# Kernel optimization log

Hardware: AMD Instinct MI355X
Metric: run time of the kernel (lower is better)

## Reference

```python
import jax, jax.numpy as jnp
import numpy as np

NUM_NODES = 1_000_000  # global node-state table size
N = 100_000            # batch of unique nodes
D = 128                # embedding dim
SIZE = 32              # map is SIZE x SIZE cells
C = SIZE * SIZE        # 1024 cells


def setup_inputs() -> dict:
    key = jax.random.key(0)
    k1, k2, k3, k4 = jax.random.split(key, 4)
    embeddings = jax.random.normal(k1, (N, D), dtype=jnp.float32)
    memory_map = jax.random.normal(k2, (C, D), dtype=jnp.float32)
    nodes = jax.random.randint(k3, (N,), 0, NUM_NODES, dtype=jnp.int64)
    times = jax.random.uniform(k4, (N,), dtype=jnp.float32)
    # node state tables: cell assignment initialized to -1 (unassigned), time to 0
    node_cell = jnp.full((NUM_NODES,), -1, dtype=jnp.int32)
    node_time = jnp.zeros((NUM_NODES,), dtype=jnp.float32)
    return {"embeddings": embeddings, "memory_map": memory_map,
            "nodes": nodes, "times": times,
            "node_cell": node_cell, "node_time": node_time}


def _euclidean_cdist(x, m):
    # torch.cdist(x, m, p=2): [N, C] pairwise L2 distances
    sq = (jnp.sum(x * x, axis=1, keepdims=True)
          + jnp.sum(m * m, axis=1)[None, :]
          - 2.0 * (x @ m.T))
    return jnp.sqrt(jnp.maximum(sq, 0.0))


def reference(embeddings, memory_map, nodes, times, node_cell, node_time):
    # find_center_distances: distance of each node embedding to every map cell,
    # nearest-cell assignment, then scatter update of the node state tables
    # (memory_map.set_nodes_distance(nodes, cells, times)).
    distances = _euclidean_cdist(embeddings, memory_map)      # [N, C]
    min_indices = jnp.argmin(distances, axis=1)               # [N]
    cells = min_indices.astype(jnp.int32)                     # list_num[min_indices] == min_indices
    new_node_cell = node_cell.at[nodes].set(cells)
    new_node_time = node_time.at[nodes].set(times)
    return distances, cells, new_node_cell, new_node_time
```

## Files before the change

### kernel.cpp

```cpp
#include <hip/hip_runtime.h>
#include <stdint.h>

constexpr int D_DIM   = 128;
constexpr int C_CELLS = 1024;
constexpr float EPS_D = 1.5e-3f;

typedef __attribute__((ext_vector_type(8))) short  short8;
typedef __attribute__((ext_vector_type(4))) float  floatx4;

#define GLOBAL_AS __attribute__((address_space(1)))
#define LDS_AS    __attribute__((address_space(3)))

__device__ __forceinline__ void gl2lds16(const void* g, void* l) {
    __builtin_amdgcn_global_load_lds((const GLOBAL_AS unsigned int*)g,
                                     (LDS_AS unsigned int*)l, 16, 0, 0);
}

__device__ __forceinline__ unsigned short f32_bf16_rtn(float x) {
    union { float f; unsigned u; } v; v.f = x;
    unsigned r = v.u + 0x7FFFu + ((v.u >> 16) & 1u);
    return (unsigned short)(r >> 16);
}
__device__ __forceinline__ float bf16_f32(unsigned short h) {
    union { float f; unsigned u; } v; v.u = ((unsigned)h) << 16; return v.f;
}
__device__ __forceinline__ float hi_f32(unsigned long long p) {
    union { float f; unsigned u; } v; v.u = (unsigned)(p >> 32); return v.f;
}

__global__ void init_kernel(int* win, int* flag, int* suspCount, int numNodes) {
    int j = blockIdx.x * blockDim.x + threadIdx.x;
    if (j < numNodes) win[j] = -1;
    if (j == 0) { *flag = 1; *suspCount = 0; }
}

__global__ void detect_kernel(const int* nodes32, int n, int* flag) {
    int i = blockIdx.x * blockDim.x + threadIdx.x;
    if (i < n && (i & 1) && nodes32[i] != 0) *flag = 0;
}

__global__ void winner_kernel(const void* nodes, int n, const int* flag, int* win) {
    int i = blockIdx.x * blockDim.x + threadIdx.x;
    if (i >= n) return;
    int node = (*flag) ? (int)((const long long*)nodes)[i]
                       : ((const int*)nodes)[i];
    atomicMax(&win[node], i);
}

__global__ void norms_kernel(const float* __restrict__ v, float* __restrict__ o, int rows) {
    int row  = blockIdx.x * 4 + (threadIdx.x >> 6);
    int lane = threadIdx.x & 63;
    if (row >= rows) return;
    float2 x = reinterpret_cast<const float2*>(v)[(size_t)row * 64 + lane];
    float s = x.x * x.x + x.y * x.y;
    #pragma unroll
    for (int m = 32; m; m >>= 1) s += __shfl_xor(s, m, 64);
    if (lane == 0) o[row] = s;
}

__global__ void convB_kernel(const float* __restrict__ M,
                             unsigned short* __restrict__ Bh_g,
                             unsigned short* __restrict__ Bl_g) {
    int idx  = blockIdx.x * 256 + threadIdx.x;
    int cell = idx >> 4;
    int b    = idx & 15;
    const float4* s = reinterpret_cast<const float4*>(M + (size_t)cell * D_DIM + b * 8);
    float4 v0 = s[0], v1 = s[1];
    float xv[8] = { v0.x, v0.y, v0.z, v0.w, v1.x, v1.y, v1.z, v1.w };
    short8 hs, ls;
    #pragma unroll
    for (int j = 0; j < 8; ++j) {
        unsigned short hb = f32_bf16_rtn(xv[j]);
        unsigned short lb = f32_bf16_rtn(xv[j] - bf16_f32(hb));
        hs[j] = (short)hb; ls[j] = (short)lb;
    }
    int tile = cell >> 6, r = cell & 63;
    int dst = tile * 8192 + r * 128 + ((b ^ (r & 15)) << 3);
    *reinterpret_cast<short8*>(&Bh_g[dst]) = hs;
    *reinterpret_cast<short8*>(&Bl_g[dst]) = ls;
}

__global__ __launch_bounds__(256, 2)
void dist_kernel(const float* __restrict__ X,
                 const unsigned short* __restrict__ Bh_g,
                 const unsigned short* __restrict__ Bl_g,
                 const float* __restrict__ msq,
                 float* __restrict__ outD, int* __restrict__ cells32,
                 int* __restrict__ suspects, int* __restrict__ suspCount,
                 int N)
{
    __shared__ __align__(16) unsigned short Ah[64 * 128];
    __shared__ __align__(16) unsigned short Al[64 * 128];
    __shared__ __align__(16) unsigned short Bh[64 * 128];
    __shared__ __align__(16) unsigned short Bl[64 * 128];
    __shared__ float Axs[64];
    __shared__ unsigned long long sp1[64][2];
    __shared__ float              sm2[64][2];

    const int tid  = threadIdx.x;
    const int lane = tid & 63;
    const int wave = tid >> 6;
    const int q    = lane >> 4;
    const int l15  = lane & 15;
    const int w0   = wave & 1;
    const int w1   = wave >> 1;
    const int blockRow = blockIdx.x * 64;

    #pragma unroll
    for (int p = 0; p < 4; ++p) {
        int r = p * 16 + (tid >> 4);
        int b = tid & 15;
        int gRow = blockRow + r;
        float4 v0 = make_float4(0.f, 0.f, 0.f, 0.f), v1 = v0;
        if (gRow < N) {
            const float4* s = reinterpret_cast<const float4*>(X + (size_t)gRow * D_DIM + b * 8);
            v0 = s[0]; v1 = s[1];
        }
        float xv[8] = { v0.x, v0.y, v0.z, v0.w, v1.x, v1.y, v1.z, v1.w };
        short8 hs, ls;
        float sq = 0.f;
        #pragma unroll
        for (int j = 0; j < 8; ++j) {
            sq += xv[j] * xv[j];
            unsigned short hb = f32_bf16_rtn(xv[j]);
            unsigned short lb = f32_bf16_rtn(xv[j] - bf16_f32(hb));
            hs[j] = (short)hb; ls[j] = (short)lb;
        }
        #pragma unroll
        for (int m = 1; m < 16; m <<= 1) sq += __shfl_xor(sq, m, 16);
        if (b == 0) Axs[r] = sq;
        int ad = r * 128 + ((b ^ (r & 15)) << 3);
        *reinterpret_cast<short8*>(&Ah[ad]) = hs;
        *reinterpret_cast<short8*>(&Al[ad]) = ls;
    }
    __syncthreads();

    float xs[8];
    #pragma unroll
    for (int t = 0; t < 2; ++t)
        #pragma unroll
        for (int r = 0; r < 4; ++r)
            xs[t * 4 + r] = Axs[w1 * 32 + t * 16 + q * 4 + r];

    float rminv[8]; float rmin2[8]; int rminc[8];
    #pragma unroll
    for (int i = 0; i < 8; ++i) { rminv[i] = INFINITY; rmin2[i] = INFINITY; rminc[i] = 0; }

    for (int ct = 0; ct < 16; ++ct) {
        if (ct) __syncthreads();
        {
            const char* bhg = (const char*)Bh_g + (size_t)ct * 16384 + wave * 4096 + lane * 16;
            const char* blg = (const char*)Bl_g + (size_t)ct * 16384 + wave * 4096 + lane * 16;
            char* bhl = (char*)Bh + wave * 4096;
            char* bll = (char*)Bl + wave * 4096;
            #pragma unroll
            for (int j = 0; j < 4; ++j) {
                gl2lds16(bhg + j * 1024, bhl + j * 1024);
                gl2lds16(blg + j * 1024, bll + j * 1024);
            }
        }
        __syncthreads();

        floatx4 acc[2][2];
        #pragma unroll
        for (int t = 0; t < 2; ++t)
            #pragma unroll
            for (int u = 0; u < 2; ++u)
                acc[t][u] = (floatx4){0.f, 0.f, 0.f, 0.f};

        #pragma unroll
        for (int kc = 0; kc < 4; ++kc) {
            int blk = kc * 4 + q;
            short8 ah[2], al[2], bh[2], bl[2];
            #pragma unroll
            for (int t = 0; t < 2; ++t) {
                int row = w1 * 32 + t * 16 + l15;
                int ad  = row * 128 + ((blk ^ l15) << 3);
                ah[t] = *reinterpret_cast<const short8*>(&Ah[ad]);
                al[t] = *reinterpret_cast<const short8*>(&Al[ad]);
            }
            #pragma unroll
            for (int u = 0; u < 2; ++u) {
                int col = w0 * 32 + u * 16 + l15;
                int ad  = col * 128 + ((blk ^ l15) << 3);
                bh[u] = *reinterpret_cast<const short8*>(&Bh[ad]);
                bl[u] = *reinterpret_cast<const short8*>(&Bl[ad]);
            }
            #pragma unroll
            for (int t = 0; t < 2; ++t)
                #pragma unroll
                for (int u = 0; u < 2; ++u) {
                    acc[t][u] = __builtin_amdgcn_mfma_f32_16x16x32_bf16(ah[t], bh[u], acc[t][u], 0, 0, 0);
                    acc[t][u] = __builtin_amdgcn_mfma_f32_16x16x32_bf16(ah[t], bl[u], acc[t][u], 0, 0, 0);
                    acc[t][u] = __builtin_amdgcn_mfma_f32_16x16x32_bf16(al[t], bh[u], acc[t][u], 0, 0, 0);
                }
        }

        #pragma unroll
        for (int u = 0; u < 2; ++u) {
            int col = ct * 64 + w0 * 32 + u * 16 + l15;
            float ms = msq[col];
            #pragma unroll
            for (int t = 0; t < 2; ++t)
                #pragma unroll
                for (int r = 0; r < 4; ++r) {
                    int g  = blockRow + w1 * 32 + t * 16 + q * 4 + r;
                    int i  = t * 4 + r;
                    float sq = xs[i] + ms - 2.0f * acc[t][u][r];
                    float d  = sqrtf(fmaxf(sq, 0.0f));
                    if (g < N) __builtin_nontemporal_store(d, &outD[(size_t)g * C_CELLS + col]);
                    if (d < rminv[i]) { rmin2[i] = rminv[i]; rminv[i] = d; rminc[i] = col; }
                    else if (d < rmin2[i]) rmin2[i] = d;
                }
        }
    }

    #pragma unroll
    for (int i = 0; i < 8; ++i) {
        union { float f; unsigned u; } bu; bu.f = rminv[i];
        unsigned long long p1 = ((unsigned long long)bu.u << 32) | (unsigned)rminc[i];
        float m2 = rmin2[i];
        #pragma unroll
        for (int m = 1; m < 16; m <<= 1) {
            unsigned long long o1 = __shfl_xor(p1, m, 16);
            float o2 = __shfl_xor(m2, m, 16);
            unsigned long long hi = (p1 > o1) ? p1 : o1;
            float hv = hi_f32(hi);
            p1 = (p1 < o1) ? p1 : o1;
            m2 = fminf(fminf(m2, o2), hv);
        }
        if (l15 == 0) {
            int lr = w1 * 32 + (i >> 2) * 16 + q * 4 + (i & 3);
            sp1[lr][w0] = p1; sm2[lr][w0] = m2;
        }
    }
    __syncthreads();
    if (tid < 64) {
        int g = blockRow + tid;
        if (g < N) {
            unsigned long long a = sp1[tid][0], b = sp1[tid][1];
            unsigned long long G1 = (a < b) ? a : b;
            unsigned long long hi = (a < b) ? b : a;
            float M2  = fminf(fminf(sm2[tid][0], sm2[tid][1]), hi_f32(hi));
            float g1v = hi_f32(G1);
            cells32[g] = (int)(G1 & 0xffffffffu);
            if (M2 - g1v < EPS_D) {
                int ix = atomicAdd(suspCount, 1);
                suspects[ix] = g;
            }
        }
    }
}

__global__ __launch_bounds__(256)
void refine_kernel(const float* __restrict__ X, const float* __restrict__ M,
                   const int* __restrict__ suspects, const int* __restrict__ suspCount,
                   int* __restrict__ cells32)
{
    __shared__ double xd[128];
    __shared__ unsigned long long wres[4];
    int cnt = *suspCount;
    for (int s = blockIdx.x; s < cnt; s += gridDim.x) {
        int row = suspects[s];
        if (threadIdx.x < 128) xd[threadIdx.x] = (double)X[(size_t)row * D_DIM + threadIdx.x];
        __syncthreads();
        unsigned long long best = ~0ull;
        for (int c = threadIdx.x; c < C_CELLS; c += 256) {
            const float* mp = M + (size_t)c * D_DIM;
            double acc = 0.0;
            #pragma unroll 4
            for (int k = 0; k < D_DIM; ++k) {
                double diff = xd[k] - (double)mp[k];
                acc = fma(diff, diff, acc);
            }
            unsigned long long bits = (unsigned long long)__double_as_longlong(acc);
            unsigned long long pk = (bits & ~1023ull) | (unsigned long long)c;
            if (pk < best) best = pk;
        }
        #pragma unroll
        for (int m = 32; m; m >>= 1) {
            unsigned long long o = __shfl_xor(best, m, 64);
            if (o < best) best = o;
        }
        if ((threadIdx.x & 63) == 0) wres[threadIdx.x >> 6] = best;
        __syncthreads();
        if (threadIdx.x == 0) {
            unsigned long long b0 = wres[0] < wres[1] ? wres[0] : wres[1];
            unsigned long long b1 = wres[2] < wres[3] ? wres[2] : wres[3];
            unsigned long long b  = b0 < b1 ? b0 : b1;
            cells32[row] = (int)(b & 1023ull);
        }
        __syncthreads();
    }
}

__global__ void post_kernel(const int* __restrict__ cells32,
                            const int* __restrict__ win,
                            const float* __restrict__ times,
                            const int* __restrict__ node_cell,
                            const float* __restrict__ node_time,
                            float* __restrict__ outCells,
                            float* __restrict__ outNC,
                            float* __restrict__ outNT,
                            int n, int numNodes)
{
    int j = blockIdx.x * blockDim.x + threadIdx.x;
    if (j < n) outCells[j] = (float)cells32[j];
    if (j < numNodes) {
        int w = win[j];
        float c, t;
        if (w >= 0) {
            c = (float)cells32[w];
            t = times[w];
        } else {
            c = (float)node_cell[j];
            t = node_time[j];
        }
        outNC[j] = c;
        outNT[j] = t;
    }
}

extern "C" void kernel_launch(void* const* d_in, const int* in_sizes, int n_in,
                              void* d_out, int out_size, void* d_ws, size_t ws_size,
                              hipStream_t stream)
{
    const float* X         = (const float*)d_in[0];
    const float* M         = (const float*)d_in[1];
    const void*  nodes     = d_in[2];
    const float* times     = (const float*)d_in[3];
    const int*   node_cell = (const int*)d_in[4];
    const float* node_time = (const float*)d_in[5];

    const int N        = in_sizes[3];
    const int numNodes = in_sizes[4];
    const int C        = in_sizes[1] / D_DIM;

    char* ws = (char*)d_ws;
    size_t off = 0;
    unsigned short* Bh_g = (unsigned short*)(ws + off); off += (size_t)C * D_DIM * 2;
    unsigned short* Bl_g = (unsigned short*)(ws + off); off += (size_t)C * D_DIM * 2;
    int* win      = (int*)(ws + off); off += (size_t)numNodes * 4;
    int* cells32  = (int*)(ws + off); off += (size_t)N * 4;
    int* suspects = (int*)(ws + off); off += (size_t)N * 4;
    float* msq    = (float*)(ws + off); off += (size_t)C * 4;
    int* flag     = (int*)(ws + off); off += 4;
    int* suspCount= (int*)(ws + off); off += 4;
    (void)ws_size; (void)n_in; (void)out_size;

    float* outD     = (float*)d_out;
    float* outCells = outD + (size_t)N * C;
    float* outNC    = outCells + N;
    float* outNT    = outNC + numNodes;

    init_kernel  <<<(numNodes + 255) / 256, 256, 0, stream>>>(win, flag, suspCount, numNodes);
    detect_kernel<<<(N + 255) / 256, 256, 0, stream>>>((const int*)nodes, N, flag);
    winner_kernel<<<(N + 255) / 256, 256, 0, stream>>>(nodes, N, flag, win);
    norms_kernel <<<(C + 3) / 4, 256, 0, stream>>>(M, msq, C);
    convB_kernel <<<(C * 16 + 255) / 256, 256, 0, stream>>>(M, Bh_g, Bl_g);
    dist_kernel  <<<(N + 63) / 64, 256, 0, stream>>>(X, Bh_g, Bl_g, msq, outD, cells32,
                                                     suspects, suspCount, N);
    refine_kernel<<<512, 256, 0, stream>>>(X, M, suspects, suspCount, cells32);
    post_kernel  <<<(numNodes + 255) / 256, 256, 0, stream>>>(cells32, win, times, node_cell,
                                                              node_time, outCells, outNC, outNT,
                                                              N, numNodes);
}
```

Baseline: 717.4 us.

## Hold X fragments in registers, prefetch next map tile, vectorize distance stores

```diff
diff --git a/kernel.cpp b/kernel.cpp
--- a/kernel.cpp
+++ b/kernel.cpp
@@ -80,7 +80,7 @@
     *reinterpret_cast<short8*>(&Bl_g[dst]) = ls;
 }
 
-__global__ __launch_bounds__(256, 2)
+__global__ __launch_bounds__(256, 3)
 void dist_kernel(const float* __restrict__ X,
                  const unsigned short* __restrict__ Bh_g,
                  const unsigned short* __restrict__ Bl_g,
@@ -89,10 +89,9 @@
                  int* __restrict__ suspects, int* __restrict__ suspCount,
                  int N)
 {
-    __shared__ __align__(16) unsigned short Ah[64 * 128];
-    __shared__ __align__(16) unsigned short Al[64 * 128];
-    __shared__ __align__(16) unsigned short Bh[64 * 128];
-    __shared__ __align__(16) unsigned short Bl[64 * 128];
+    __shared__ __align__(16) unsigned short ldsH[64 * 128];
+    __shared__ __align__(16) unsigned short ldsL[64 * 128];
+    __shared__ float msq_s[C_CELLS];
     __shared__ float Axs[64];
     __shared__ unsigned long long sp1[64][2];
     __shared__ float              sm2[64][2];
@@ -105,6 +104,7 @@
     const int w0   = wave & 1;
     const int w1   = wave >> 1;
     const int blockRow = blockIdx.x * 64;
+    const bool fullBlock = (blockRow + 64 <= N);
 
     #pragma unroll
     for (int p = 0; p < 4; ++p) {
@@ -130,108 +130,149 @@
         for (int m = 1; m < 16; m <<= 1) sq += __shfl_xor(sq, m, 16);
         if (b == 0) Axs[r] = sq;
         int ad = r * 128 + ((b ^ (r & 15)) << 3);
-        *reinterpret_cast<short8*>(&Ah[ad]) = hs;
-        *reinterpret_cast<short8*>(&Al[ad]) = ls;
+        *reinterpret_cast<short8*>(&ldsH[ad]) = hs;
+        *reinterpret_cast<short8*>(&ldsL[ad]) = ls;
+    }
+    {
+        float4 mv = *reinterpret_cast<const float4*>(&msq[tid * 4]);
+        *reinterpret_cast<float4*>(&msq_s[tid * 4]) = mv;
     }
     __syncthreads();
 
-    float xs[8];
+    short8 xh[2][4], xl[2][4];
     #pragma unroll
     for (int t = 0; t < 2; ++t)
         #pragma unroll
-        for (int r = 0; r < 4; ++r)
-            xs[t * 4 + r] = Axs[w1 * 32 + t * 16 + q * 4 + r];
-
-    float rminv[8]; float rmin2[8]; int rminc[8];
-    #pragma unroll
-    for (int i = 0; i < 8; ++i) { rminv[i] = INFINITY; rmin2[i] = INFINITY; rminc[i] = 0; }
+        for (int kc = 0; kc < 4; ++kc) {
+            int row = w1 * 32 + t * 16 + l15;
+            int ad  = row * 128 + (((kc * 4 + q) ^ l15) << 3);
+            xh[t][kc] = *reinterpret_cast<const short8*>(&ldsH[ad]);
+            xl[t][kc] = *reinterpret_cast<const short8*>(&ldsL[ad]);
+        }
+    float xs[2];
+    xs[0] = Axs[w1 * 32 + l15];
+    xs[1] = Axs[w1 * 32 + 16 + l15];
+    __syncthreads();
+
+    {
+        const char* bhg = (const char*)Bh_g + wave * 4096 + lane * 16;
+        const char* blg = (const char*)Bl_g + wave * 4096 + lane * 16;
+        char* bhl = (char*)ldsH + wave * 4096;
+        char* bll = (char*)ldsL + wave * 4096;
+        #pragma unroll
+        for (int j = 0; j < 4; ++j) {
+            gl2lds16(bhg + j * 1024, bhl + j * 1024);
+            gl2lds16(blg + j * 1024, bll + j * 1024);
+        }
+    }
+    asm volatile("s_waitcnt vmcnt(0)" ::: "memory");
+    __builtin_amdgcn_sched_barrier(0);
+    __builtin_amdgcn_s_barrier();
+    __builtin_amdgcn_sched_barrier(0);
+
+    float m1[2]  = { INFINITY, INFINITY };
+    float m2v[2] = { INFINITY, INFINITY };
+    int   c1[2]  = { 0, 0 };
 
     for (int ct = 0; ct < 16; ++ct) {
-        if (ct) __syncthreads();
-        {
-            const char* bhg = (const char*)Bh_g + (size_t)ct * 16384 + wave * 4096 + lane * 16;
-            const char* blg = (const char*)Bl_g + (size_t)ct * 16384 + wave * 4096 + lane * 16;
-            char* bhl = (char*)Bh + wave * 4096;
-            char* bll = (char*)Bl + wave * 4096;
+        floatx4 acc[2][2];
+        #pragma unroll
+        for (int t = 0; t < 2; ++t)
+            #pragma unroll
+            for (int u = 0; u < 2; ++u)
+                acc[t][u] = (floatx4){0.f, 0.f, 0.f, 0.f};
+
+        #pragma unroll
+        for (int kc = 0; kc < 4; ++kc) {
+            short8 mh[2], ml[2];
+            #pragma unroll
+            for (int u = 0; u < 2; ++u) {
+                int cell = w0 * 32 + u * 16 + l15;
+                int ad   = cell * 128 + (((kc * 4 + q) ^ l15) << 3);
+                mh[u] = *reinterpret_cast<const short8*>(&ldsH[ad]);
+                ml[u] = *reinterpret_cast<const short8*>(&ldsL[ad]);
+            }
+            #pragma unroll
+            for (int t = 0; t < 2; ++t)
+                #pragma unroll
+                for (int u = 0; u < 2; ++u) {
+                    acc[t][u] = __builtin_amdgcn_mfma_f32_16x16x32_bf16(mh[u], xh[t][kc], acc[t][u], 0, 0, 0);
+                    acc[t][u] = __builtin_amdgcn_mfma_f32_16x16x32_bf16(mh[u], xl[t][kc], acc[t][u], 0, 0, 0);
+                    acc[t][u] = __builtin_amdgcn_mfma_f32_16x16x32_bf16(ml[u], xh[t][kc], acc[t][u], 0, 0, 0);
+                }
+        }
+
+        floatx4 dv[2][2];
+        #pragma unroll
+        for (int u = 0; u < 2; ++u) {
+            int cbase = ct * 64 + w0 * 32 + u * 16 + q * 4;
+            float4 ms4 = *reinterpret_cast<const float4*>(&msq_s[cbase]);
+            float msv[4] = { ms4.x, ms4.y, ms4.z, ms4.w };
+            #pragma unroll
+            for (int t = 0; t < 2; ++t) {
+                #pragma unroll
+                for (int r = 0; r < 4; ++r) {
+                    float s = fmaf(-2.0f, acc[t][u][r], xs[t] + msv[r]);
+                    dv[t][u][r] = __builtin_amdgcn_sqrtf(fmaxf(s, 0.0f));
+                    m2v[t] = __builtin_amdgcn_fmed3f(s, m1[t], m2v[t]);
+                    c1[t]  = (s < m1[t]) ? (cbase + r) : c1[t];
+                    m1[t]  = fminf(s, m1[t]);
+                }
+            }
+        }
+
+        __builtin_amdgcn_s_barrier();
+        __builtin_amdgcn_sched_barrier(0);
+        if (ct < 15) {
+            const char* bhg = (const char*)Bh_g + (size_t)(ct + 1) * 16384 + wave * 4096 + lane * 16;
+            const char* blg = (const char*)Bl_g + (size_t)(ct + 1) * 16384 + wave * 4096 + lane * 16;
+            char* bhl = (char*)ldsH + wave * 4096;
+            char* bll = (char*)ldsL + wave * 4096;
             #pragma unroll
             for (int j = 0; j < 4; ++j) {
                 gl2lds16(bhg + j * 1024, bhl + j * 1024);
                 gl2lds16(blg + j * 1024, bll + j * 1024);
             }
         }
-        __syncthreads();
-
-        floatx4 acc[2][2];
-        #pragma unroll
-        for (int t = 0; t < 2; ++t)
-            #pragma unroll
-            for (int u = 0; u < 2; ++u)
-                acc[t][u] = (floatx4){0.f, 0.f, 0.f, 0.f};
-
-        #pragma unroll
-        for (int kc = 0; kc < 4; ++kc) {
-            int blk = kc * 4 + q;
-            short8 ah[2], al[2], bh[2], bl[2];
-            #pragma unroll
-            for (int t = 0; t < 2; ++t) {
-                int row = w1 * 32 + t * 16 + l15;
-                int ad  = row * 128 + ((blk ^ l15) << 3);
-                ah[t] = *reinterpret_cast<const short8*>(&Ah[ad]);
-                al[t] = *reinterpret_cast<const short8*>(&Al[ad]);
-            }
-            #pragma unroll
-            for (int u = 0; u < 2; ++u) {
-                int col = w0 * 32 + u * 16 + l15;
-                int ad  = col * 128 + ((blk ^ l15) << 3);
-                bh[u] = *reinterpret_cast<const short8*>(&Bh[ad]);
-                bl[u] = *reinterpret_cast<const short8*>(&Bl[ad]);
-            }
-            #pragma unroll
-            for (int t = 0; t < 2; ++t)
-                #pragma unroll
-                for (int u = 0; u < 2; ++u) {
-                    acc[t][u] = __builtin_amdgcn_mfma_f32_16x16x32_bf16(ah[t], bh[u], acc[t][u], 0, 0, 0);
-                    acc[t][u] = __builtin_amdgcn_mfma_f32_16x16x32_bf16(ah[t], bl[u], acc[t][u], 0, 0, 0);
-                    acc[t][u] = __builtin_amdgcn_mfma_f32_16x16x32_bf16(al[t], bh[u], acc[t][u], 0, 0, 0);
-                }
-        }
-
-        #pragma unroll
-        for (int u = 0; u < 2; ++u) {
-            int col = ct * 64 + w0 * 32 + u * 16 + l15;
-            float ms = msq[col];
-            #pragma unroll
-            for (int t = 0; t < 2; ++t)
-                #pragma unroll
-                for (int r = 0; r < 4; ++r) {
-                    int g  = blockRow + w1 * 32 + t * 16 + q * 4 + r;
-                    int i  = t * 4 + r;
-                    float sq = xs[i] + ms - 2.0f * acc[t][u][r];
-                    float d  = sqrtf(fmaxf(sq, 0.0f));
-                    if (g < N) __builtin_nontemporal_store(d, &outD[(size_t)g * C_CELLS + col]);
-                    if (d < rminv[i]) { rmin2[i] = rminv[i]; rminv[i] = d; rminc[i] = col; }
-                    else if (d < rmin2[i]) rmin2[i] = d;
-                }
+        #pragma unroll
+        for (int t = 0; t < 2; ++t) {
+            int grow = blockRow + w1 * 32 + t * 16 + l15;
+            if (grow < N) {
+                size_t rb = (size_t)grow * C_CELLS + ct * 64 + w0 * 32 + q * 4;
+                __builtin_nontemporal_store(dv[t][0], reinterpret_cast<floatx4*>(&outD[rb]));
+                __builtin_nontemporal_store(dv[t][1], reinterpret_cast<floatx4*>(&outD[rb + 16]));
+            }
+        }
+        __builtin_amdgcn_sched_barrier(0);
+        if (ct < 15) {
+            if (fullBlock) asm volatile("s_waitcnt vmcnt(4)" ::: "memory");
+            else           asm volatile("s_waitcnt vmcnt(0)" ::: "memory");
+            __builtin_amdgcn_sched_barrier(0);
+            __builtin_amdgcn_s_barrier();
+            __builtin_amdgcn_sched_barrier(0);
         }
     }
 
     #pragma unroll
-    for (int i = 0; i < 8; ++i) {
-        union { float f; unsigned u; } bu; bu.f = rminv[i];
-        unsigned long long p1 = ((unsigned long long)bu.u << 32) | (unsigned)rminc[i];
-        float m2 = rmin2[i];
-        #pragma unroll
-        for (int m = 1; m < 16; m <<= 1) {
-            unsigned long long o1 = __shfl_xor(p1, m, 16);
-            float o2 = __shfl_xor(m2, m, 16);
-            unsigned long long hi = (p1 > o1) ? p1 : o1;
-            float hv = hi_f32(hi);
-            p1 = (p1 < o1) ? p1 : o1;
-            m2 = fminf(fminf(m2, o2), hv);
-        }
-        if (l15 == 0) {
-            int lr = w1 * 32 + (i >> 2) * 16 + q * 4 + (i & 3);
-            sp1[lr][w0] = p1; sm2[lr][w0] = m2;
+    for (int t = 0; t < 2; ++t) {
+        float a1 = m1[t], a2 = m2v[t]; int ac = c1[t];
+        #pragma unroll
+        for (int off = 16; off <= 32; off <<= 1) {
+            float b1 = __shfl_xor(a1, off, 64);
+            float b2 = __shfl_xor(a2, off, 64);
+            int   bc = __shfl_xor(ac, off, 64);
+            float hi = fmaxf(a1, b1);
+            ac = (b1 < a1) ? bc : ac;
+            a1 = fminf(a1, b1);
+            a2 = fminf(fminf(a2, b2), hi);
+        }
+        if (q == 0) {
+            int lr = w1 * 32 + t * 16 + l15;
+            float d1 = __builtin_amdgcn_sqrtf(fmaxf(a1, 0.0f));
+            float d2 = __builtin_amdgcn_sqrtf(fmaxf(a2, 0.0f));
+            union { float f; unsigned u; } bu; bu.f = d1;
+            sp1[lr][w0] = ((unsigned long long)bu.u << 32) | (unsigned)ac;
+            sm2[lr][w0] = d2;
         }
     }
     __syncthreads();
```

After: 589.5 us. 1.22x faster.
